# Kernel optimization log

Hardware: AMD Instinct MI355X
Metric: run time of the kernel (lower is better)

The kernel has to match this reference:

```python
import jax, jax.numpy as jnp
import numpy as np

B, T, C, H = 4, 2048, 1024, 16
D = C // H  # head_size = 64


def setup_inputs() -> dict:
    key = jax.random.key(0)
    k1, k2, k3 = jax.random.split(key, 3)
    s = 1.0 / np.sqrt(C)
    return {
        "x": jax.random.normal(k1, (B, T, C), dtype=jnp.float32),
        "w_qkv": jax.random.normal(k2, (3 * C, C), dtype=jnp.float32) * s,
        "w_out": jax.random.normal(k3, (C, C), dtype=jnp.float32) * s,
        "b_out": jnp.zeros((C,), dtype=jnp.float32),
    }


def reference(x, w_qkv, w_out, b_out):
    Bx, Tx, Cx = x.shape
    qkv = x @ w_qkv.T                                # [B,T,3C]
    q, k, v = jnp.split(qkv, 3, axis=2)
    # [B,T,C] -> [B,H,T,D]
    q = q.reshape(Bx, Tx, H, D).transpose(0, 2, 1, 3)
    k = k.reshape(Bx, Tx, H, D).transpose(0, 2, 1, 3)
    v = v.reshape(Bx, Tx, H, D).transpose(0, 2, 1, 3)
    scores = jnp.einsum('bhqd,bhkd->bhqk', q, k) / jnp.sqrt(jnp.float32(D))
    causal = jnp.tril(jnp.ones((Tx, Tx), dtype=bool))
    scores = jnp.where(causal[None, None], scores, -jnp.inf)
    attn = jax.nn.softmax(scores, axis=-1)
    out = jnp.einsum('bhqk,bhkd->bhqd', attn, v)     # [B,H,T,D]
    out = out.transpose(0, 2, 1, 3).reshape(Bx, Tx, Cx)
    return out @ w_out.T + b_out
```

## Files before the change

kernel.cpp:

```cpp
#include <hip/hip_runtime.h>

constexpr int Bn = 4, Tn = 2048, Cn = 1024, Hn = 16, Dn = 64;

typedef __attribute__((ext_vector_type(8))) short short8;
typedef __attribute__((ext_vector_type(4))) float floatx4;
typedef __attribute__((ext_vector_type(2))) unsigned uint2v;
typedef __attribute__((ext_vector_type(4))) unsigned uint4v;

#define DEVFN __device__ __forceinline__

constexpr float SCL = 0.18033688011112042f;

DEVFN unsigned f2bf_u(float f) {
  unsigned u = __builtin_bit_cast(unsigned, f);
  u += 0x7fffu + ((u >> 16) & 1u);
  return u >> 16;
}
DEVFN short f2bf(float f) { return (short)f2bf_u(f); }

DEVFN unsigned cvtpk(float lo, float hi) {
  unsigned r;
  asm("v_cvt_pk_bf16_f32 %0, %1, %2" : "=v"(r) : "v"(lo), "v"(hi));
  return r;
}

DEVFN floatx4 mfma16(short8 a, short8 b, floatx4 c) {
  return __builtin_amdgcn_mfma_f32_16x16x32_bf16(a, b, c, 0, 0, 0);
}

DEVFN void gld_lds16(const void* g, void* l) {
  __builtin_amdgcn_global_load_lds(
      (const __attribute__((address_space(1))) unsigned*)g,
      (__attribute__((address_space(3))) unsigned*)l, 16, 0, 0);
}

constexpr int G_X = 8192 * 1024 / 8;
constexpr int G_WQ = 3072 * 1024 / 8;
constexpr int G_WO = 1024 * 1024 / 8;
__global__ __launch_bounds__(256) void cast3_kernel(
    const float* __restrict__ x, const float* __restrict__ wq,
    const float* __restrict__ wo, short* __restrict__ dst) {
  const int i = blockIdx.x * 256 + threadIdx.x;
  const float* src;
  int rel;
  if (i < G_X) {
    src = x; rel = i;
  } else if (i < G_X + G_WQ) {
    src = wq; rel = i - G_X;
  } else {
    src = wo; rel = i - (G_X + G_WQ);
  }
  const floatx4* p = (const floatx4*)src + (size_t)rel * 2;
  floatx4 a = p[0], b = p[1];
  uint4v r;
  r[0] = cvtpk(a[0], a[1]);
  r[1] = cvtpk(a[2], a[3]);
  r[2] = cvtpk(b[0], b[1]);
  r[3] = cvtpk(b[2], b[3]);
  ((uint4v*)dst)[i] = r;
}

template <int MODE>
__global__ __launch_bounds__(256, 2) void gemm_bt(
    const short* __restrict__ A, const short* __restrict__ Bw, int M, int N, int K,
    short* __restrict__ qkb, short* __restrict__ vtb,
    const float* __restrict__ bias, float* __restrict__ fout) {
  __shared__ short As[128 * 64];
  __shared__ short Bs[128 * 64];
  const int tid = threadIdx.x;
  const int lane = tid & 63, wave = tid >> 6;
  const int l15 = lane & 15, quad = lane >> 4;
  const int wr = wave >> 1, wc = wave & 1;
  const int m0 = blockIdx.x * 128, n0 = blockIdx.y * 128;

  const int r0 = tid >> 3, cs = tid & 7;
  const short* Ag = A + (size_t)(m0 + r0) * K + (cs ^ (r0 & 7)) * 8;
  const short* Bg = Bw + (size_t)(n0 + r0) * K + (cs ^ (r0 & 7)) * 8;

  floatx4 acc[4][4] = {};

  for (int k0 = 0; k0 < K; k0 += 64) {
#pragma unroll
    for (int it = 0; it < 4; ++it) {
      gld_lds16(Ag + k0 + (size_t)(it * 32) * K, As + it * 2048 + tid * 8);
      gld_lds16(Bg + k0 + (size_t)(it * 32) * K, Bs + it * 2048 + tid * 8);
    }
    __syncthreads();
#pragma unroll
    for (int ks = 0; ks < 2; ++ks) {
      short8 af[4], bf[4];
#pragma unroll
      for (int i = 0; i < 4; ++i) {
        const int row = wr * 64 + i * 16 + l15;
        af[i] = *(const short8*)(As + row * 64 +
                                 ((ks * 4 + quad) ^ (l15 & 7)) * 8);
      }
#pragma unroll
      for (int i = 0; i < 4; ++i) {
        const int row = wc * 64 + i * 16 + l15;
        bf[i] = *(const short8*)(Bs + row * 64 +
                                 ((ks * 4 + quad) ^ (l15 & 7)) * 8);
      }
#pragma unroll
      for (int mi = 0; mi < 4; ++mi)
#pragma unroll
        for (int ni = 0; ni < 4; ++ni)
          acc[mi][ni] = mfma16(af[mi], bf[ni], acc[mi][ni]);
    }
    __syncthreads();
  }

#pragma unroll
  for (int mi = 0; mi < 4; ++mi) {
    const int row0 = m0 + wr * 64 + mi * 16 + quad * 4;
#pragma unroll
    for (int ni = 0; ni < 4; ++ni) {
      const int col = n0 + wc * 64 + ni * 16 + l15;
      if constexpr (MODE == 0) {
        if (col < 2 * Cn) {
#pragma unroll
          for (int r = 0; r < 4; ++r) {
            float v = acc[mi][ni][r];
            if (col < Cn) v *= SCL;
            qkb[(size_t)(row0 + r) * (2 * Cn) + col] = f2bf(v);
          }
        } else {
          const int hc = col - 2 * Cn;
          const int hh = hc >> 6, d = hc & 63;
          const int bb = row0 >> 11, t = row0 & (Tn - 1);
          uint2v pk;
          pk[0] = cvtpk(acc[mi][ni][0], acc[mi][ni][1]);
          pk[1] = cvtpk(acc[mi][ni][2], acc[mi][ni][3]);
          *(uint2v*)(vtb + ((size_t)((bb * Hn + hh) * Dn + d)) * Tn + t) = pk;
        }
      } else {
#pragma unroll
        for (int r = 0; r < 4; ++r)
          fout[(size_t)(row0 + r) * N + col] = acc[mi][ni][r] + bias[col];
      }
    }
  }
}

__global__ __launch_bounds__(256, 3) void attn_kernel(
    const short* __restrict__ qk, const short* __restrict__ vt,
    short* __restrict__ att) {
  __shared__ short Ks[2][64 * 64];
  __shared__ short Vs[2][64 * 64];
  __shared__ short Ps[4][16 * 64];

  const int bh = blockIdx.x;
  const int qt =
      (int)((0x32104567ba98cdefULL >> (blockIdx.y * 4)) & 0xFULL);
  const int b = bh >> 4, h = bh & 15;
  const int tid = threadIdx.x;
  const int lane = tid & 63, wave = tid >> 6;
  const int l15 = lane & 15, quad = lane >> 4;
  const int q0w = qt * 128 + wave * 32;

  const short* qbase = qk + (size_t)(b * Tn) * 2048 + h * 64;
  const short* kbase = qbase + 1024;
  const short* vbase = vt + (size_t)(bh * 64) * Tn;
  short* pw = Ps[wave];

  short8 qf[2][2];
#pragma unroll
  for (int f = 0; f < 2; ++f)
#pragma unroll
    for (int ks = 0; ks < 2; ++ks)
      qf[f][ks] = *(const short8*)(qbase + (size_t)(q0w + f * 16 + l15) * 2048 +
                                   ks * 32 + quad * 8);

  short8 ones;
#pragma unroll
  for (int i = 0; i < 8; ++i) ones[i] = (short)0x3F80;

  floatx4 o[2][4] = {};
  floatx4 sum_acc[2] = {};

  const int wave_nt = ((q0w + 31) >> 6) + 1;
  const int block_nt = 2 * qt + 2;

  const int jr = tid >> 3;
  const int cl = tid & 7;

#define STAGE(JT, BUF)                                                       \
  {                                                                          \
    const int j0s = (JT) * 64;                                               \
    _Pragma("unroll") for (int it = 0; it < 2; ++it) {                       \
      const int row = jr + it * 32;                                          \
      const int cg = cl ^ (row & 7);                                         \
      gld_lds16(kbase + (size_t)(j0s + row) * 2048 + cg * 8,                 \
                &Ks[BUF][it * 2048 + tid * 8]);                              \
      gld_lds16(vbase + (size_t)row * Tn + j0s + cg * 8,                     \
                &Vs[BUF][it * 2048 + tid * 8]);                              \
    }                                                                        \
  }

  STAGE(0, 0)
  __syncthreads();

  for (int jt = 0; jt < block_nt; ++jt) {
    const int buf = jt & 1;
    if (jt + 1 < block_nt) STAGE(jt + 1, buf ^ 1)

    if (jt < wave_nt) {
      const int j0 = jt * 64;

      floatx4 st[2][4];
#pragma unroll
      for (int f = 0; f < 2; ++f)
#pragma unroll
        for (int nj = 0; nj < 4; ++nj) st[f][nj] = floatx4{0.f, 0.f, 0.f, 0.f};
#pragma unroll
      for (int half = 0; half < 2; ++half) {
        short8 kfa[2][2];
#pragma unroll
        for (int j2 = 0; j2 < 2; ++j2)
#pragma unroll
          for (int ks = 0; ks < 2; ++ks) {
            const int cld = (ks * 4 + quad) ^ (l15 & 7);
            kfa[j2][ks] = *(const short8*)(
                &Ks[buf][((half * 2 + j2) * 16 + l15) * 64 + cld * 8]);
          }
        __builtin_amdgcn_s_setprio(1);
#pragma unroll
        for (int f = 0; f < 2; ++f)
#pragma unroll
          for (int j2 = 0; j2 < 2; ++j2)
#pragma unroll
            for (int ks = 0; ks < 2; ++ks)
              st[f][half * 2 + j2] =
                  mfma16(kfa[j2][ks], qf[f][ks], st[f][half * 2 + j2]);
        __builtin_amdgcn_s_setprio(0);
      }

      short8 vf[4][2];
#pragma unroll
      for (int nd = 0; nd < 4; ++nd)
#pragma unroll
        for (int ks = 0; ks < 2; ++ks) {
          const int cld = (ks * 4 + quad) ^ (l15 & 7);
          vf[nd][ks] =
              *(const short8*)(&Vs[buf][(nd * 16 + l15) * 64 + cld * 8]);
        }

#pragma unroll
      for (int f = 0; f < 2; ++f) {
        const bool need_mask = (j0 + 63 > q0w + f * 16);
        const int ig = q0w + f * 16 + l15;
#pragma unroll
        for (int nj = 0; nj < 4; ++nj) {
          float p[4];
#pragma unroll
          for (int r = 0; r < 4; ++r) {
            float e = __builtin_amdgcn_exp2f(st[f][nj][r]);
            if (need_mask) {
              const int jg = j0 + nj * 16 + quad * 4 + r;
              e = (jg > ig) ? 0.f : e;
            }
            p[r] = e;
          }
          const int c = nj * 2 + (quad >> 1);
          const int cld = c ^ (l15 & 7);
          uint2v pk;
          pk[0] = cvtpk(p[0], p[1]);
          pk[1] = cvtpk(p[2], p[3]);
          *(uint2v*)(&pw[l15 * 64 + cld * 8 + (quad & 1) * 4]) = pk;
        }
        __asm__ volatile("s_waitcnt lgkmcnt(0)" ::: "memory");

        short8 pf[2];
#pragma unroll
        for (int ks = 0; ks < 2; ++ks) {
          const int cld = (ks * 4 + quad) ^ (l15 & 7);
          pf[ks] = *(const short8*)(&pw[l15 * 64 + cld * 8]);
        }
        __builtin_amdgcn_s_setprio(1);
#pragma unroll
        for (int nd = 0; nd < 4; ++nd)
#pragma unroll
          for (int ks = 0; ks < 2; ++ks)
            o[f][nd] = mfma16(vf[nd][ks], pf[ks], o[f][nd]);
#pragma unroll
        for (int ks = 0; ks < 2; ++ks)
          sum_acc[f] = mfma16(ones, pf[ks], sum_acc[f]);
        __builtin_amdgcn_s_setprio(0);
        __asm__ volatile("" ::: "memory");
      }
    }
    __syncthreads();
  }

  float inv[2];
#pragma unroll
  for (int f = 0; f < 2; ++f) inv[f] = 1.0f / sum_acc[f][0];

#pragma unroll
  for (int f = 0; f < 2; ++f) {
#pragma unroll
    for (int nd = 0; nd < 4; ++nd) {
      const int c = nd * 2 + (quad >> 1);
      const int cld = c ^ (l15 & 7);
      uint2v pk;
      pk[0] = cvtpk(o[f][nd][0] * inv[f], o[f][nd][1] * inv[f]);
      pk[1] = cvtpk(o[f][nd][2] * inv[f], o[f][nd][3] * inv[f]);
      *(uint2v*)(&pw[l15 * 64 + cld * 8 + (quad & 1) * 4]) = pk;
    }
    __asm__ volatile("s_waitcnt lgkmcnt(0)" ::: "memory");
#pragma unroll
    for (int ps = 0; ps < 2; ++ps) {
      const int r16 = ps * 8 + (lane >> 3);
      const int cn = lane & 7;
      const int cldr = cn ^ (r16 & 7);
      const short8 val = *(const short8*)(&pw[r16 * 64 + cldr * 8]);
      *(short8*)(att + (size_t)(b * Tn + q0w + f * 16 + r16) * Cn + h * 64 +
                 cn * 8) = val;
    }
    __asm__ volatile("" ::: "memory");
  }
#undef STAGE
}

extern "C" void kernel_launch(void* const* d_in, const int* in_sizes, int n_in,
                              void* d_out, int out_size, void* d_ws,
                              size_t ws_size, hipStream_t stream) {
  const float* x = (const float*)d_in[0];
  const float* w_qkv = (const float*)d_in[1];
  const float* w_out = (const float*)d_in[2];
  const float* b_out = (const float*)d_in[3];
  float* out = (float*)d_out;

  short* xb = (short*)d_ws;
  short* wqb = xb + (size_t)8192 * 1024;
  short* wob = wqb + (size_t)3072 * 1024;
  short* qkb = wob + (size_t)1024 * 1024;
  short* vtb = qkb + (size_t)8192 * 2048;
  short* att = xb;

  cast3_kernel<<<dim3((G_X + G_WQ + G_WO) / 256), 256, 0, stream>>>(
      x, w_qkv, w_out, xb);

  gemm_bt<0><<<dim3(64, 24), 256, 0, stream>>>(xb, wqb, 8192, 3072, 1024, qkb,
                                               vtb, nullptr, nullptr);
  attn_kernel<<<dim3(64, 16), 256, 0, stream>>>(qkb, vtb, att);
  gemm_bt<1><<<dim3(64, 8), 256, 0, stream>>>(att, wob, 8192, 1024, 1024,
                                              nullptr, nullptr, b_out, out);
}
```

Measured before the change: 224.8 us.

## Shrink attention query tile to 64 rows per block with one fragment per wave

The attention kernel now gives each block 64 query rows instead of 128, so each wave handles 16 query rows rather than 32. The grid doubles to 32 query tiles, ordered longest-first. Per-wave key-range skipping and the two-fragment inner loop are removed, which cuts register pressure and causal imbalance and raises block count. In exchange, every K/V tile is staged into shared memory twice as often across blocks, and each staged tile feeds half as many MFMAs.

```diff
diff --git a/kernel.cpp b/kernel.cpp
--- a/kernel.cpp
+++ b/kernel.cpp
@@ -150,36 +150,32 @@
   __shared__ short Ps[4][16 * 64];
 
   const int bh = blockIdx.x;
-  const int qt =
-      (int)((0x32104567ba98cdefULL >> (blockIdx.y * 4)) & 0xFULL);
+  const int qh = 31 - blockIdx.y;
   const int b = bh >> 4, h = bh & 15;
   const int tid = threadIdx.x;
   const int lane = tid & 63, wave = tid >> 6;
   const int l15 = lane & 15, quad = lane >> 4;
-  const int q0w = qt * 128 + wave * 32;
+  const int q0w = qh * 64 + wave * 16;
 
   const short* qbase = qk + (size_t)(b * Tn) * 2048 + h * 64;
   const short* kbase = qbase + 1024;
   const short* vbase = vt + (size_t)(bh * 64) * Tn;
   short* pw = Ps[wave];
 
-  short8 qf[2][2];
-#pragma unroll
-  for (int f = 0; f < 2; ++f)
-#pragma unroll
-    for (int ks = 0; ks < 2; ++ks)
-      qf[f][ks] = *(const short8*)(qbase + (size_t)(q0w + f * 16 + l15) * 2048 +
-                                   ks * 32 + quad * 8);
+  short8 qf[2];
+#pragma unroll
+  for (int ks = 0; ks < 2; ++ks)
+    qf[ks] = *(const short8*)(qbase + (size_t)(q0w + l15) * 2048 + ks * 32 +
+                              quad * 8);
 
   short8 ones;
 #pragma unroll
   for (int i = 0; i < 8; ++i) ones[i] = (short)0x3F80;
 
-  floatx4 o[2][4] = {};
-  floatx4 sum_acc[2] = {};
-
-  const int wave_nt = ((q0w + 31) >> 6) + 1;
-  const int block_nt = 2 * qt + 2;
+  floatx4 o[4] = {};
+  floatx4 sum_acc = {};
+
+  const int block_nt = qh + 1;
 
   const int jr = tid >> 3;
   const int cl = tid & 7;
@@ -202,122 +198,105 @@
 
   for (int jt = 0; jt < block_nt; ++jt) {
     const int buf = jt & 1;
+    const int j0 = jt * 64;
     if (jt + 1 < block_nt) STAGE(jt + 1, buf ^ 1)
 
-    if (jt < wave_nt) {
-      const int j0 = jt * 64;
-
-      floatx4 st[2][4];
-#pragma unroll
-      for (int f = 0; f < 2; ++f)
-#pragma unroll
-        for (int nj = 0; nj < 4; ++nj) st[f][nj] = floatx4{0.f, 0.f, 0.f, 0.f};
-#pragma unroll
-      for (int half = 0; half < 2; ++half) {
-        short8 kfa[2][2];
-#pragma unroll
-        for (int j2 = 0; j2 < 2; ++j2)
-#pragma unroll
-          for (int ks = 0; ks < 2; ++ks) {
-            const int cld = (ks * 4 + quad) ^ (l15 & 7);
-            kfa[j2][ks] = *(const short8*)(
-                &Ks[buf][((half * 2 + j2) * 16 + l15) * 64 + cld * 8]);
-          }
-        __builtin_amdgcn_s_setprio(1);
-#pragma unroll
-        for (int f = 0; f < 2; ++f)
-#pragma unroll
-          for (int j2 = 0; j2 < 2; ++j2)
-#pragma unroll
-            for (int ks = 0; ks < 2; ++ks)
-              st[f][half * 2 + j2] =
-                  mfma16(kfa[j2][ks], qf[f][ks], st[f][half * 2 + j2]);
-        __builtin_amdgcn_s_setprio(0);
-      }
-
-      short8 vf[4][2];
-#pragma unroll
-      for (int nd = 0; nd < 4; ++nd)
+    floatx4 st[4];
+#pragma unroll
+    for (int nj = 0; nj < 4; ++nj) st[nj] = floatx4{0.f, 0.f, 0.f, 0.f};
+#pragma unroll
+    for (int half = 0; half < 2; ++half) {
+      short8 kfa[2][2];
+#pragma unroll
+      for (int j2 = 0; j2 < 2; ++j2)
 #pragma unroll
         for (int ks = 0; ks < 2; ++ks) {
           const int cld = (ks * 4 + quad) ^ (l15 & 7);
-          vf[nd][ks] =
-              *(const short8*)(&Vs[buf][(nd * 16 + l15) * 64 + cld * 8]);
+          kfa[j2][ks] = *(const short8*)(
+              &Ks[buf][((half * 2 + j2) * 16 + l15) * 64 + cld * 8]);
         }
-
-#pragma unroll
-      for (int f = 0; f < 2; ++f) {
-        const bool need_mask = (j0 + 63 > q0w + f * 16);
-        const int ig = q0w + f * 16 + l15;
-#pragma unroll
-        for (int nj = 0; nj < 4; ++nj) {
-          float p[4];
-#pragma unroll
-          for (int r = 0; r < 4; ++r) {
-            float e = __builtin_amdgcn_exp2f(st[f][nj][r]);
-            if (need_mask) {
-              const int jg = j0 + nj * 16 + quad * 4 + r;
-              e = (jg > ig) ? 0.f : e;
-            }
-            p[r] = e;
-          }
-          const int c = nj * 2 + (quad >> 1);
-          const int cld = c ^ (l15 & 7);
-          uint2v pk;
-          pk[0] = cvtpk(p[0], p[1]);
-          pk[1] = cvtpk(p[2], p[3]);
-          *(uint2v*)(&pw[l15 * 64 + cld * 8 + (quad & 1) * 4]) = pk;
+      __builtin_amdgcn_s_setprio(1);
+#pragma unroll
+      for (int j2 = 0; j2 < 2; ++j2)
+#pragma unroll
+        for (int ks = 0; ks < 2; ++ks)
+          st[half * 2 + j2] = mfma16(kfa[j2][ks], qf[ks], st[half * 2 + j2]);
+      __builtin_amdgcn_s_setprio(0);
+    }
+
+    short8 vf[4][2];
+#pragma unroll
+    for (int nd = 0; nd < 4; ++nd)
+#pragma unroll
+      for (int ks = 0; ks < 2; ++ks) {
+        const int cld = (ks * 4 + quad) ^ (l15 & 7);
+        vf[nd][ks] =
+            *(const short8*)(&Vs[buf][(nd * 16 + l15) * 64 + cld * 8]);
+      }
+
+    const bool need_mask = (j0 + 63 > q0w);
+    const int ig = q0w + l15;
+#pragma unroll
+    for (int nj = 0; nj < 4; ++nj) {
+      float p[4];
+#pragma unroll
+      for (int r = 0; r < 4; ++r) {
+        float e = __builtin_amdgcn_exp2f(st[nj][r]);
+        if (need_mask) {
+          const int jg = j0 + nj * 16 + quad * 4 + r;
+          e = (jg > ig) ? 0.f : e;
         }
-        __asm__ volatile("s_waitcnt lgkmcnt(0)" ::: "memory");
-
-        short8 pf[2];
-#pragma unroll
-        for (int ks = 0; ks < 2; ++ks) {
-          const int cld = (ks * 4 + quad) ^ (l15 & 7);
-          pf[ks] = *(const short8*)(&pw[l15 * 64 + cld * 8]);
-        }
-        __builtin_amdgcn_s_setprio(1);
-#pragma unroll
-        for (int nd = 0; nd < 4; ++nd)
-#pragma unroll
-          for (int ks = 0; ks < 2; ++ks)
-            o[f][nd] = mfma16(vf[nd][ks], pf[ks], o[f][nd]);
-#pragma unroll
-        for (int ks = 0; ks < 2; ++ks)
-          sum_acc[f] = mfma16(ones, pf[ks], sum_acc[f]);
-        __builtin_amdgcn_s_setprio(0);
-        __asm__ volatile("" ::: "memory");
-      }
-    }
-    __syncthreads();
-  }
-
-  float inv[2];
-#pragma unroll
-  for (int f = 0; f < 2; ++f) inv[f] = 1.0f / sum_acc[f][0];
-
-#pragma unroll
-  for (int f = 0; f < 2; ++f) {
-#pragma unroll
-    for (int nd = 0; nd < 4; ++nd) {
-      const int c = nd * 2 + (quad >> 1);
+        p[r] = e;
+      }
+      const int c = nj * 2 + (quad >> 1);
       const int cld = c ^ (l15 & 7);
       uint2v pk;
-      pk[0] = cvtpk(o[f][nd][0] * inv[f], o[f][nd][1] * inv[f]);
-      pk[1] = cvtpk(o[f][nd][2] * inv[f], o[f][nd][3] * inv[f]);
+      pk[0] = cvtpk(p[0], p[1]);
+      pk[1] = cvtpk(p[2], p[3]);
       *(uint2v*)(&pw[l15 * 64 + cld * 8 + (quad & 1) * 4]) = pk;
     }
     __asm__ volatile("s_waitcnt lgkmcnt(0)" ::: "memory");
-#pragma unroll
-    for (int ps = 0; ps < 2; ++ps) {
-      const int r16 = ps * 8 + (lane >> 3);
-      const int cn = lane & 7;
-      const int cldr = cn ^ (r16 & 7);
-      const short8 val = *(const short8*)(&pw[r16 * 64 + cldr * 8]);
-      *(short8*)(att + (size_t)(b * Tn + q0w + f * 16 + r16) * Cn + h * 64 +
-                 cn * 8) = val;
-    }
+
+    short8 pf[2];
+#pragma unroll
+    for (int ks = 0; ks < 2; ++ks) {
+      const int cld = (ks * 4 + quad) ^ (l15 & 7);
+      pf[ks] = *(const short8*)(&pw[l15 * 64 + cld * 8]);
+    }
+    __builtin_amdgcn_s_setprio(1);
+#pragma unroll
+    for (int nd = 0; nd < 4; ++nd)
+#pragma unroll
+      for (int ks = 0; ks < 2; ++ks)
+        o[nd] = mfma16(vf[nd][ks], pf[ks], o[nd]);
+#pragma unroll
+    for (int ks = 0; ks < 2; ++ks) sum_acc = mfma16(ones, pf[ks], sum_acc);
+    __builtin_amdgcn_s_setprio(0);
     __asm__ volatile("" ::: "memory");
+
+    __syncthreads();
+  }
+
+  const float inv = 1.0f / sum_acc[0];
+
+#pragma unroll
+  for (int nd = 0; nd < 4; ++nd) {
+    const int c = nd * 2 + (quad >> 1);
+    const int cld = c ^ (l15 & 7);
+    uint2v pk;
+    pk[0] = cvtpk(o[nd][0] * inv, o[nd][1] * inv);
+    pk[1] = cvtpk(o[nd][2] * inv, o[nd][3] * inv);
+    *(uint2v*)(&pw[l15 * 64 + cld * 8 + (quad & 1) * 4]) = pk;
+  }
+  __asm__ volatile("s_waitcnt lgkmcnt(0)" ::: "memory");
+#pragma unroll
+  for (int ps = 0; ps < 2; ++ps) {
+    const int r16 = ps * 8 + (lane >> 3);
+    const int cn = lane & 7;
+    const int cldr = cn ^ (r16 & 7);
+    const short8 val = *(const short8*)(&pw[r16 * 64 + cldr * 8]);
+    *(short8*)(att + (size_t)(b * Tn + q0w + r16) * Cn + h * 64 + cn * 8) =
+        val;
   }
 #undef STAGE
 }
@@ -343,7 +322,7 @@
 
   gemm_bt<0><<<dim3(64, 24), 256, 0, stream>>>(xb, wqb, 8192, 3072, 1024, qkb,
                                                vtb, nullptr, nullptr);
-  attn_kernel<<<dim3(64, 16), 256, 0, stream>>>(qkb, vtb, att);
+  attn_kernel<<<dim3(64, 32), 256, 0, stream>>>(qkb, vtb, att);
   gemm_bt<1><<<dim3(64, 8), 256, 0, stream>>>(att, wob, 8192, 1024, 1024,
                                               nullptr, nullptr, b_out, out);
 }
```

New measurement: 227.3 us. About the same (+1.1%).
